# Kernel optimization log

Hardware: AMD Instinct MI355X
Metric: run time of the kernel (lower is better)

## Reference

```python
import jax, jax.numpy as jnp
import numpy as np

N_NODES = 100000

def spmm(rows, cols, vals, x):
    # out[r] = sum_e vals[e] * x[cols[e]] for edges with rows[e] == r
    msgs = vals[:, None] * x[cols]            # [E, F]
    return jax.ops.segment_sum(msgs, rows, num_segments=N_NODES)

def setup_inputs() -> dict:
    key = jax.random.key(0)
    ks = jax.random.split(key, 8)
    N, E, F_IN, H, C = N_NODES, 1600000, 128, 128, 64
    x = jax.random.normal(ks[0], (N, F_IN), dtype=jnp.float32)
    edge_rows = jax.random.randint(ks[1], (E,), 0, N, dtype=jnp.int32)
    edge_cols = jax.random.randint(ks[2], (E,), 0, N, dtype=jnp.int32)
    edge_vals = jax.random.uniform(ks[3], (E,), dtype=jnp.float32)
    W1 = jax.random.normal(ks[4], (F_IN, H), dtype=jnp.float32) * (1.0 / np.sqrt(F_IN))
    b1 = jnp.zeros((H,), dtype=jnp.float32)
    W2 = jax.random.normal(ks[5], (H, C), dtype=jnp.float32) * (1.0 / np.sqrt(H))
    b2 = jnp.zeros((C,), dtype=jnp.float32)
    return {"x": x, "edge_rows": edge_rows, "edge_cols": edge_cols,
            "edge_vals": edge_vals, "W1": W1, "b1": b1, "W2": W2, "b2": b2}

def reference(x, edge_rows, edge_cols, edge_vals, W1, b1, W2, b2):
    # Layer 1: spmm(adj, x) then linear, then ReLU (dropout = identity at eval)
    h = spmm(edge_rows, edge_cols, edge_vals, x)   # [N, F_IN]
    h = h @ W1 + b1                                # [N, H]
    h = jax.nn.relu(h)
    # Layer 2
    h = spmm(edge_rows, edge_cols, edge_vals, h)   # [N, H]
    return h @ W2 + b2                             # [N, C]
```

## Files before the change

### kernel.cpp

```cpp
#include <hip/hip_runtime.h>


typedef __attribute__((ext_vector_type(8))) short short8;
typedef __attribute__((ext_vector_type(4))) float floatx4;
typedef __attribute__((ext_vector_type(2))) float floatx2;

#define ELLS 64
#define RW   256
#define CH   4096
#define EPT  16
#define MAXB 400
#define SLP  68

static __device__ __forceinline__ unsigned short f2bf(float f) {
    unsigned int u = __builtin_bit_cast(unsigned int, f);
    u += 0x7fffu + ((u >> 16) & 1u);
    return (unsigned short)(u >> 16);
}
static __device__ __forceinline__ float bflo(unsigned int u) {
    return __builtin_bit_cast(float, u << 16);
}
static __device__ __forceinline__ float bfhi(unsigned int u) {
    return __builtin_bit_cast(float, u & 0xffff0000u);
}
static __device__ __forceinline__ float slotval(unsigned int s) {
    return (float)(s >> 17) * (1.0f / 32767.0f);
}

__global__ __launch_bounds__(256) void prep_kernel(
    const float* __restrict__ W1, const float* __restrict__ W2,
    unsigned short* __restrict__ W1t, unsigned short* __restrict__ W2t)
{
    int idx = blockIdx.x * 256 + threadIdx.x;
    if (idx < 128 * 128) {
        int n = idx >> 7, k = idx & 127;
        W1t[idx] = f2bf(W1[(size_t)k * 128 + n]);
    }
    if (idx < 64 * 128) {
        int n = idx >> 7, k = idx & 127;
        W2t[idx] = f2bf(W2[(size_t)k * 64 + n]);
    }
}

static __device__ __forceinline__ void gemm1_body(
    const float* __restrict__ A, const unsigned short* __restrict__ Wt,
    unsigned short* __restrict__ Ys, int NP, int N, int bid)
{
    const int lane = threadIdx.x & 63;
    const int wave = threadIdx.x >> 6;
    const int quad = lane >> 4;
    const int l16  = lane & 15;
    const int row0 = bid * 64 + wave * 16;
    int arow = row0 + l16;
    if (arow > N - 1) arow = N - 1;

    short8 af[4];
    const float* ap = A + (size_t)arow * 128 + quad * 8;
    #pragma unroll
    for (int kt = 0; kt < 4; ++kt) {
        const floatx4* p = (const floatx4*)(ap + kt * 32);
        floatx4 lo = __builtin_nontemporal_load(p);
        floatx4 hi = __builtin_nontemporal_load(p + 1);
        short8 t;
        t[0] = (short)f2bf(lo[0]); t[1] = (short)f2bf(lo[1]);
        t[2] = (short)f2bf(lo[2]); t[3] = (short)f2bf(lo[3]);
        t[4] = (short)f2bf(hi[0]); t[5] = (short)f2bf(hi[1]);
        t[6] = (short)f2bf(hi[2]); t[7] = (short)f2bf(hi[3]);
        af[kt] = t;
    }

    floatx4 acc[8];
    #pragma unroll
    for (int nt = 0; nt < 8; ++nt) acc[nt] = (floatx4){0.f, 0.f, 0.f, 0.f};

    #pragma unroll
    for (int nt = 0; nt < 8; ++nt) {
        const unsigned short* wp = Wt + (size_t)(nt * 16 + l16) * 128 + quad * 8;
        #pragma unroll
        for (int kt = 0; kt < 4; ++kt) {
            short8 bfr = *(const short8*)(wp + kt * 32);
            acc[nt] = __builtin_amdgcn_mfma_f32_16x16x32_bf16(
                af[kt], bfr, acc[nt], 0, 0, 0);
        }
    }

    #pragma unroll
    for (int nt = 0; nt < 8; ++nt) {
        #pragma unroll
        for (int r = 0; r < 4; ++r) {
            int row = row0 + quad * 4 + r;
            if (row < N)
                Ys[(size_t)nt * NP * 16 + (size_t)row * 16 + l16] =
                    f2bf(acc[nt][r]);
        }
    }
}

__global__ __launch_bounds__(256) void binA_gemm1_fused(
    const int* __restrict__ erow, const int* __restrict__ ecol,
    const float* __restrict__ eval,
    uint2* __restrict__ slab, unsigned int* __restrict__ offsT,
    int E, int NC, int NB,
    const float* __restrict__ x, const unsigned short* __restrict__ W1t,
    unsigned short* __restrict__ y1s, int NP, int N)
{
    __shared__ unsigned int hist[MAXB + 1];
    __shared__ uint2 compact[CH];

    if ((int)blockIdx.x < NC) {
        const int t     = threadIdx.x;
        const int chunk = blockIdx.x;

        for (int i = t; i <= NB; i += 256) hist[i] = 0;
        __syncthreads();

        int base = chunk * CH + t * EPT;
        unsigned int w0[EPT];
        unsigned int vb[EPT];
        int bk[EPT], rk[EPT];

        if (base + EPT <= E) {
            #pragma unroll
            for (int q = 0; q < 4; ++q) {
                int4   r4 = *(const int4*)(erow + base + q * 4);
                int4   c4 = *(const int4*)(ecol + base + q * 4);
                float4 v4 = *(const float4*)(eval + base + q * 4);
                int rr[4]   = {r4.x, r4.y, r4.z, r4.w};
                int cc[4]   = {c4.x, c4.y, c4.z, c4.w};
                float vv[4] = {v4.x, v4.y, v4.z, v4.w};
                #pragma unroll
                for (int j = 0; j < 4; ++j) {
                    int i = q * 4 + j;
                    bk[i] = rr[j] >> 8;
                    w0[i] = (unsigned int)cc[j]
                          | (((unsigned int)rr[j] & (RW - 1)) << 17);
                    vb[i] = __builtin_bit_cast(unsigned int, vv[j]);
                }
            }
        } else {
            #pragma unroll
            for (int j = 0; j < EPT; ++j) {
                int e = base + j;
                if (e < E) {
                    int r = erow[e];
                    bk[j] = r >> 8;
                    w0[j] = (unsigned int)ecol[e]
                          | (((unsigned int)r & (RW - 1)) << 17);
                    vb[j] = __builtin_bit_cast(unsigned int, eval[e]);
                } else {
                    bk[j] = NB;
                    w0[j] = 0u; vb[j] = 0u;
                }
            }
        }

        #pragma unroll
        for (int j = 0; j < EPT; ++j)
            rk[j] = (int)atomicAdd(&hist[bk[j]], 1u);
        __syncthreads();

        if (t == 0) {
            unsigned int run = 0;
            for (int i = 0; i <= NB; ++i) {
                unsigned int c = hist[i];
                hist[i] = run;
                run += c;
            }
        }
        __syncthreads();

        #pragma unroll
        for (int j = 0; j < EPT; ++j) {
            unsigned int pos = hist[bk[j]] + (unsigned int)rk[j];
            uint2 e; e.x = w0[j]; e.y = vb[j];
            compact[pos] = e;
        }
        __syncthreads();

        uint2* sp = slab + (size_t)chunk * CH;
        #pragma unroll
        for (int s = 0; s < EPT; ++s)
            sp[s * 256 + t] = compact[s * 256 + t];
        unsigned int* op = offsT + (size_t)chunk * (NB + 1);
        for (int i = t; i <= NB; i += 256) op[i] = hist[i];
    } else {
        gemm1_body(x, W1t, y1s, NP, N, blockIdx.x - NC);
    }
}

__global__ __launch_bounds__(256) void binB(
    const uint2* __restrict__ slab, const unsigned int* __restrict__ offsT,
    unsigned int* __restrict__ ell, int* __restrict__ deg,
    int NC, int NB, int N)
{
    __shared__ unsigned int ell_lds[RW * ELLS];
    __shared__ unsigned int cur[RW];

    const int t = threadIdx.x;
    const int b = blockIdx.x;

    for (int i = t; i < RW; i += 256) cur[i] = 0;
    __syncthreads();

    const int grp = t >> 5;
    const int sl  = t & 31;
    for (int cbase = 0; cbase < NC; cbase += 8) {
        int c = cbase + grp;
        if (c < NC) {
            const unsigned int* op = offsT + (size_t)c * (NB + 1) + b;
            unsigned int off = op[0];
            unsigned int end = op[1];
            const uint2* sp = slab + (size_t)c * CH;
            for (unsigned int i = off + (unsigned)sl; i < end; i += 32) {
                uint2 e = sp[i];
                unsigned int rin = e.x >> 17;
                unsigned int col = e.x & 0x1FFFFu;
                float v = __builtin_bit_cast(float, e.y);
                unsigned int q = (unsigned int)(int)(v * 32767.f + 0.5f);
                unsigned int p = atomicAdd(&cur[rin], 1u);
                if (p < ELLS)
                    ell_lds[rin * ELLS + p] = col | (q << 17);
            }
        }
    }
    __syncthreads();

    const uint4* src = (const uint4*)ell_lds;
    uint4* dst = (uint4*)(ell + (size_t)b * RW * ELLS);
    #pragma unroll
    for (int s = 0; s < (RW * ELLS / 4) / 256; ++s)
        dst[s * 256 + t] = src[s * 256 + t];

    int row = b * RW + t;
    if (row < N) deg[row] = min((int)cur[t], ELLS);
}

__global__ __launch_bounds__(256) void spmm1_sliced(
    const int* __restrict__ deg, const unsigned int* __restrict__ ell,
    const unsigned short* __restrict__ y1s, const float* __restrict__ b1,
    unsigned short* __restrict__ h2s, int NP, int N)
{
    __shared__ unsigned int slds[4 * 16 * SLP];

    const int slice = blockIdx.x & 7;
    const int rblk  = blockIdx.x >> 3;
    const int wave  = threadIdx.x >> 6;
    const int lane  = threadIdx.x & 63;
    const int r     = lane >> 2;
    const int fl    = lane & 3;
    const int rbase = rblk * 64 + wave * 16;
    const int row   = rbase + r;

    unsigned int* sw = slds + wave * (16 * SLP);
    const uint4* gp = (const uint4*)(ell + (size_t)rbase * ELLS);
    #pragma unroll
    for (int t = 0; t < 4; ++t) {
        uint4 q = gp[t * 64 + lane];
        int linear = t * 256 + lane * 4;
        int rr = linear >> 6, ii = linear & 63;
        *(uint4*)(sw + rr * SLP + ii) = q;
    }

    int rc = (row < N) ? row : 0;
    int d  = deg[rc];
    if (row >= N) d = 0;

    int dm = d;
    dm = max(dm, __shfl_xor(dm, 4));
    dm = max(dm, __shfl_xor(dm, 8));
    dm = max(dm, __shfl_xor(dm, 16));
    dm = max(dm, __shfl_xor(dm, 32));
    int dm4 = (dm + 3) & ~3;

    const unsigned int* xu = (const unsigned int*)y1s + (size_t)slice * NP * 8;
    const unsigned int* sr = sw + r * SLP;
    float a0 = 0.f, a1 = 0.f, a2 = 0.f, a3 = 0.f;

    for (int i = 0; i < dm4; i += 4) {
        uint4 q = *(const uint4*)(sr + i);
        unsigned int s[4] = {q.x, q.y, q.z, q.w};
        uint2 u[4];
        #pragma unroll
        for (int j = 0; j < 4; ++j) {
            s[j] = (i + j < d) ? s[j] : 0u;
            u[j] = *((const uint2*)(xu + (s[j] & 0x1FFFFu) * 8) + fl);
        }
        #pragma unroll
        for (int j = 0; j < 4; ++j) {
            float v = slotval(s[j]);
            a0 = fmaf(v, bflo(u[j].x), a0);
            a1 = fmaf(v, bfhi(u[j].x), a1);
            a2 = fmaf(v, bflo(u[j].y), a2);
            a3 = fmaf(v, bfhi(u[j].y), a3);
        }
    }

    if (row < N) {
        float4 b = ((const float4*)b1)[slice * 4 + fl];
        unsigned int p0 = (unsigned int)f2bf(fmaxf(a0 + b.x, 0.f))
                        | ((unsigned int)f2bf(fmaxf(a1 + b.y, 0.f)) << 16);
        unsigned int p1 = (unsigned int)f2bf(fmaxf(a2 + b.z, 0.f))
                        | ((unsigned int)f2bf(fmaxf(a3 + b.w, 0.f)) << 16);
        uint2 o; o.x = p0; o.y = p1;
        *(uint2*)((unsigned int*)h2s + (size_t)slice * NP * 8
                  + (size_t)row * 8 + fl * 2) = o;
    }
}

__global__ __launch_bounds__(256) void gemm2_kernel(
    const unsigned short* __restrict__ h2s,
    const unsigned short* __restrict__ W2t,
    unsigned short* __restrict__ y2s, int NP, int N)
{
    const int lane = threadIdx.x & 63;
    const int wave = threadIdx.x >> 6;
    const int quad = lane >> 4;
    const int l16  = lane & 15;
    const int row0 = blockIdx.x * 64 + wave * 16;
    int arow = row0 + l16;
    if (arow > N - 1) arow = N - 1;

    short8 af[4];
    #pragma unroll
    for (int kt = 0; kt < 4; ++kt) {
        int slice = kt * 2 + (quad >> 1);
        af[kt] = *(const short8*)(h2s + (size_t)slice * NP * 16
                                  + (size_t)arow * 16 + (quad & 1) * 8);
    }

    floatx4 acc[4];
    #pragma unroll
    for (int nt = 0; nt < 4; ++nt) acc[nt] = (floatx4){0.f, 0.f, 0.f, 0.f};

    #pragma unroll
    for (int nt = 0; nt < 4; ++nt) {
        const unsigned short* wp = W2t + (size_t)(nt * 16 + l16) * 128 + quad * 8;
        #pragma unroll
        for (int kt = 0; kt < 4; ++kt) {
            short8 bfr = *(const short8*)(wp + kt * 32);
            acc[nt] = __builtin_amdgcn_mfma_f32_16x16x32_bf16(
                af[kt], bfr, acc[nt], 0, 0, 0);
        }
    }

    #pragma unroll
    for (int nt = 0; nt < 4; ++nt) {
        #pragma unroll
        for (int r = 0; r < 4; ++r) {
            int row = row0 + quad * 4 + r;
            if (row < N)
                y2s[(size_t)nt * NP * 16 + (size_t)row * 16 + l16] =
                    f2bf(acc[nt][r]);
        }
    }
}

__global__ __launch_bounds__(256) void spmm2_sliced(
    const int* __restrict__ deg, const unsigned int* __restrict__ ell,
    const unsigned short* __restrict__ y2s, const float* __restrict__ b2,
    float* __restrict__ out, int NP, int N)
{
    __shared__ unsigned int slds[4 * 16 * SLP];

    const int slice = blockIdx.x & 3;
    const int rblk  = blockIdx.x >> 2;
    const int wave  = threadIdx.x >> 6;
    const int lane  = threadIdx.x & 63;
    const int r     = lane >> 2;
    const int fl    = lane & 3;
    const int rbase = rblk * 64 + wave * 16;
    const int row   = rbase + r;

    unsigned int* sw = slds + wave * (16 * SLP);
    const uint4* gp = (const uint4*)(ell + (size_t)rbase * ELLS);
    #pragma unroll
    for (int t = 0; t < 4; ++t) {
        uint4 q = gp[t * 64 + lane];
        int linear = t * 256 + lane * 4;
        int rr = linear >> 6, ii = linear & 63;
        *(uint4*)(sw + rr * SLP + ii) = q;
    }

    int rc = (row < N) ? row : 0;
    int d  = deg[rc];
    if (row >= N) d = 0;

    int dm = d;
    dm = max(dm, __shfl_xor(dm, 4));
    dm = max(dm, __shfl_xor(dm, 8));
    dm = max(dm, __shfl_xor(dm, 16));
    dm = max(dm, __shfl_xor(dm, 32));
    int dm4 = (dm + 3) & ~3;

    const unsigned int* xu = (const unsigned int*)y2s + (size_t)slice * NP * 8;
    const unsigned int* sr = sw + r * SLP;
    float a0 = 0.f, a1 = 0.f, a2 = 0.f, a3 = 0.f;

    for (int i = 0; i < dm4; i += 4) {
        uint4 q = *(const uint4*)(sr + i);
        unsigned int s[4] = {q.x, q.y, q.z, q.w};
        uint2 u[4];
        #pragma unroll
        for (int j = 0; j < 4; ++j) {
            s[j] = (i + j < d) ? s[j] : 0u;
            u[j] = *((const uint2*)(xu + (s[j] & 0x1FFFFu) * 8) + fl);
        }
        #pragma unroll
        for (int j = 0; j < 4; ++j) {
            float v = slotval(s[j]);
            a0 = fmaf(v, bflo(u[j].x), a0);
            a1 = fmaf(v, bfhi(u[j].x), a1);
            a2 = fmaf(v, bflo(u[j].y), a2);
            a3 = fmaf(v, bfhi(u[j].y), a3);
        }
    }

    if (row < N) {
        float4 b = ((const float4*)b2)[slice * 4 + fl];
        floatx4 o;
        o[0] = a0 + b.x; o[1] = a1 + b.y; o[2] = a2 + b.z; o[3] = a3 + b.w;
        __builtin_nontemporal_store(
            o, (floatx4*)(out + (size_t)row * 64 + slice * 16 + fl * 4));
    }
}

extern "C" void kernel_launch(void* const* d_in, const int* in_sizes, int n_in,
                              void* d_out, int out_size, void* d_ws, size_t ws_size,
                              hipStream_t stream)
{
    const float* x    = (const float*)d_in[0];
    const int*   erow = (const int*)  d_in[1];
    const int*   ecol = (const int*)  d_in[2];
    const float* eval = (const float*)d_in[3];
    const float* W1   = (const float*)d_in[4];
    const float* b1   = (const float*)d_in[5];
    const float* W2   = (const float*)d_in[6];
    const float* b2   = (const float*)d_in[7];
    float*       out  = (float*)d_out;

    const int N = in_sizes[0] / 128;
    const int E = in_sizes[1];
    const int NP = N + 128;
    const int NB = (N + RW - 1) / RW;
    const int NC = (E + CH - 1) / CH;

    unsigned short* y1s = (unsigned short*)d_ws;
    unsigned short* h2s = y1s + (size_t)NP * 128;
    unsigned short* W1t = h2s + (size_t)NP * 128;
    unsigned short* W2t = W1t + 128 * 128;
    unsigned int* ell   = (unsigned int*)(W2t + 64 * 128);
    uint2* slab         = (uint2*)(ell + (size_t)NB * RW * ELLS);
    unsigned int* offsT = (unsigned int*)(slab + (size_t)NC * CH);
    int* deg            = (int*)(offsT + (size_t)NC * (NB + 1));
    unsigned short* y2s = (unsigned short*)slab;

    const int mfma_blocks = (N + 63) / 64;
    const int prep_blocks = (128 * 128 + 255) / 256;
    const int rtiles      = (N + 63) / 64;
    const int s1_blocks   = rtiles * 8;
    const int s2_blocks   = rtiles * 4;

    prep_kernel<<<prep_blocks, 256, 0, stream>>>(W1, W2, W1t, W2t);

    binA_gemm1_fused<<<NC + mfma_blocks, 256, 0, stream>>>(
        erow, ecol, eval, slab, offsT, E, NC, NB, x, W1t, y1s, NP, N);

    binB<<<NB, 256, 0, stream>>>(slab, offsT, ell, deg, NC, NB, N);

    spmm1_sliced<<<s1_blocks, 256, 0, stream>>>(
        deg, ell, y1s, b1, h2s, NP, N);

    gemm2_kernel<<<mfma_blocks, 256, 0, stream>>>(h2s, W2t, y2s, NP, N);

    spmm2_sliced<<<s2_blocks, 256, 0, stream>>>(
        deg, ell, y2s, b2, out, NP, N);
}
```

Baseline: 328.1 us.

## Store ELL in interleaved 16-row groups and precompute per-group max degree

binB now writes the ELL slots in a layout where, for each group of 16 rows, the 4-slot blocks of all 16 rows sit next to each other. An LDS bank swizzle keeps the transposing copy conflict-free. binB also writes the per-group maximum degree, so the SpMM kernels can read their index vectors straight from global memory with coalesced uint4 loads. This removes the LDS staging, the full 64-slot preload and the shuffle reductions. In exchange, index loads are now issued inside the loop rather than prefetched, and dmax needs extra workspace after deg.

```diff
diff --git a/kernel.cpp b/kernel.cpp
--- a/kernel.cpp
+++ b/kernel.cpp
@@ -10,7 +10,6 @@
 #define CH   4096
 #define EPT  16
 #define MAXB 400
-#define SLP  68
 
 static __device__ __forceinline__ unsigned short f2bf(float f) {
     unsigned int u = __builtin_bit_cast(unsigned int, f);
@@ -191,7 +190,7 @@
 __global__ __launch_bounds__(256) void binB(
     const uint2* __restrict__ slab, const unsigned int* __restrict__ offsT,
     unsigned int* __restrict__ ell, int* __restrict__ deg,
-    int NC, int NB, int N)
+    int* __restrict__ dmax, int NC, int NB, int N)
 {
     __shared__ unsigned int ell_lds[RW * ELLS];
     __shared__ unsigned int cur[RW];
@@ -218,71 +217,65 @@
                 float v = __builtin_bit_cast(float, e.y);
                 unsigned int q = (unsigned int)(int)(v * 32767.f + 0.5f);
                 unsigned int p = atomicAdd(&cur[rin], 1u);
-                if (p < ELLS)
-                    ell_lds[rin * ELLS + p] = col | (q << 17);
+                if (p < ELLS) {
+                    unsigned int blk = ((p >> 2) + rin) & 15u;
+                    ell_lds[rin * ELLS + blk * 4 + (p & 3)] = col | (q << 17);
+                }
             }
         }
     }
     __syncthreads();
 
-    const uint4* src = (const uint4*)ell_lds;
     uint4* dst = (uint4*)(ell + (size_t)b * RW * ELLS);
-    #pragma unroll
-    for (int s = 0; s < (RW * ELLS / 4) / 256; ++s)
-        dst[s * 256 + t] = src[s * 256 + t];
+    const int s4 = t >> 4;
+    const int r  = t & 15;
+    #pragma unroll
+    for (int s = 0; s < 16; ++s) {
+        unsigned int sblk = (unsigned)((s4 + r) & 15);
+        uint4 q = *(const uint4*)(ell_lds + ((s * 16 + r) * ELLS + sblk * 4));
+        dst[s * 256 + s4 * 16 + r] = q;
+    }
 
     int row = b * RW + t;
     if (row < N) deg[row] = min((int)cur[t], ELLS);
+    if (t < 16) {
+        int m = 0;
+        #pragma unroll
+        for (int i = 0; i < 16; ++i)
+            m = max(m, (int)cur[t * 16 + i]);
+        dmax[b * 16 + t] = min(m, ELLS);
+    }
 }
 
 __global__ __launch_bounds__(256) void spmm1_sliced(
-    const int* __restrict__ deg, const unsigned int* __restrict__ ell,
+    const int* __restrict__ deg, const int* __restrict__ dmax,
+    const unsigned int* __restrict__ ell,
     const unsigned short* __restrict__ y1s, const float* __restrict__ b1,
     unsigned short* __restrict__ h2s, int NP, int N)
 {
-    __shared__ unsigned int slds[4 * 16 * SLP];
-
     const int slice = blockIdx.x & 7;
     const int rblk  = blockIdx.x >> 3;
     const int wave  = threadIdx.x >> 6;
     const int lane  = threadIdx.x & 63;
     const int r     = lane >> 2;
     const int fl    = lane & 3;
-    const int rbase = rblk * 64 + wave * 16;
-    const int row   = rbase + r;
-
-    unsigned int* sw = slds + wave * (16 * SLP);
-    const uint4* gp = (const uint4*)(ell + (size_t)rbase * ELLS);
-    #pragma unroll
-    for (int t = 0; t < 4; ++t) {
-        uint4 q = gp[t * 64 + lane];
-        int linear = t * 256 + lane * 4;
-        int rr = linear >> 6, ii = linear & 63;
-        *(uint4*)(sw + rr * SLP + ii) = q;
-    }
-
-    int rc = (row < N) ? row : 0;
-    int d  = deg[rc];
-    if (row >= N) d = 0;
-
-    int dm = d;
-    dm = max(dm, __shfl_xor(dm, 4));
-    dm = max(dm, __shfl_xor(dm, 8));
-    dm = max(dm, __shfl_xor(dm, 16));
-    dm = max(dm, __shfl_xor(dm, 32));
-    int dm4 = (dm + 3) & ~3;
-
+    const int g     = rblk * 4 + wave;
+    const int row   = g * 16 + r;
+
+    int d  = (row < N) ? deg[row] : 0;
+    int nb = (dmax[g] + 3) >> 2;
+
+    const uint4* eg = (const uint4*)ell + (size_t)g * 256;
     const unsigned int* xu = (const unsigned int*)y1s + (size_t)slice * NP * 8;
-    const unsigned int* sr = sw + r * SLP;
+
     float a0 = 0.f, a1 = 0.f, a2 = 0.f, a3 = 0.f;
-
-    for (int i = 0; i < dm4; i += 4) {
-        uint4 q = *(const uint4*)(sr + i);
+    for (int i4 = 0; i4 < nb; ++i4) {
+        uint4 q = eg[i4 * 16 + r];
         unsigned int s[4] = {q.x, q.y, q.z, q.w};
         uint2 u[4];
         #pragma unroll
         for (int j = 0; j < 4; ++j) {
-            s[j] = (i + j < d) ? s[j] : 0u;
+            s[j] = (i4 * 4 + j < d) ? s[j] : 0u;
             u[j] = *((const uint2*)(xu + (s[j] & 0x1FFFFu) * 8) + fl);
         }
         #pragma unroll
@@ -356,53 +349,34 @@
 }
 
 __global__ __launch_bounds__(256) void spmm2_sliced(
-    const int* __restrict__ deg, const unsigned int* __restrict__ ell,
+    const int* __restrict__ deg, const int* __restrict__ dmax,
+    const unsigned int* __restrict__ ell,
     const unsigned short* __restrict__ y2s, const float* __restrict__ b2,
     float* __restrict__ out, int NP, int N)
 {
-    __shared__ unsigned int slds[4 * 16 * SLP];
-
     const int slice = blockIdx.x & 3;
     const int rblk  = blockIdx.x >> 2;
     const int wave  = threadIdx.x >> 6;
     const int lane  = threadIdx.x & 63;
     const int r     = lane >> 2;
     const int fl    = lane & 3;
-    const int rbase = rblk * 64 + wave * 16;
-    const int row   = rbase + r;
-
-    unsigned int* sw = slds + wave * (16 * SLP);
-    const uint4* gp = (const uint4*)(ell + (size_t)rbase * ELLS);
-    #pragma unroll
-    for (int t = 0; t < 4; ++t) {
-        uint4 q = gp[t * 64 + lane];
-        int linear = t * 256 + lane * 4;
-        int rr = linear >> 6, ii = linear & 63;
-        *(uint4*)(sw + rr * SLP + ii) = q;
-    }
-
-    int rc = (row < N) ? row : 0;
-    int d  = deg[rc];
-    if (row >= N) d = 0;
-
-    int dm = d;
-    dm = max(dm, __shfl_xor(dm, 4));
-    dm = max(dm, __shfl_xor(dm, 8));
-    dm = max(dm, __shfl_xor(dm, 16));
-    dm = max(dm, __shfl_xor(dm, 32));
-    int dm4 = (dm + 3) & ~3;
-
+    const int g     = rblk * 4 + wave;
+    const int row   = g * 16 + r;
+
+    int d  = (row < N) ? deg[row] : 0;
+    int nb = (dmax[g] + 3) >> 2;
+
+    const uint4* eg = (const uint4*)ell + (size_t)g * 256;
     const unsigned int* xu = (const unsigned int*)y2s + (size_t)slice * NP * 8;
-    const unsigned int* sr = sw + r * SLP;
+
     float a0 = 0.f, a1 = 0.f, a2 = 0.f, a3 = 0.f;
-
-    for (int i = 0; i < dm4; i += 4) {
-        uint4 q = *(const uint4*)(sr + i);
+    for (int i4 = 0; i4 < nb; ++i4) {
+        uint4 q = eg[i4 * 16 + r];
         unsigned int s[4] = {q.x, q.y, q.z, q.w};
         uint2 u[4];
         #pragma unroll
         for (int j = 0; j < 4; ++j) {
-            s[j] = (i + j < d) ? s[j] : 0u;
+            s[j] = (i4 * 4 + j < d) ? s[j] : 0u;
             u[j] = *((const uint2*)(xu + (s[j] & 0x1FFFFu) * 8) + fl);
         }
         #pragma unroll
@@ -452,6 +426,7 @@
     uint2* slab         = (uint2*)(ell + (size_t)NB * RW * ELLS);
     unsigned int* offsT = (unsigned int*)(slab + (size_t)NC * CH);
     int* deg            = (int*)(offsT + (size_t)NC * (NB + 1));
+    int* dmax           = deg + N;
     unsigned short* y2s = (unsigned short*)slab;
 
     const int mfma_blocks = (N + 63) / 64;
@@ -465,13 +440,13 @@
     binA_gemm1_fused<<<NC + mfma_blocks, 256, 0, stream>>>(
         erow, ecol, eval, slab, offsT, E, NC, NB, x, W1t, y1s, NP, N);
 
-    binB<<<NB, 256, 0, stream>>>(slab, offsT, ell, deg, NC, NB, N);
+    binB<<<NB, 256, 0, stream>>>(slab, offsT, ell, deg, dmax, NC, NB, N);
 
     spmm1_sliced<<<s1_blocks, 256, 0, stream>>>(
-        deg, ell, y1s, b1, h2s, NP, N);
+        deg, dmax, ell, y1s, b1, h2s, NP, N);
 
     gemm2_kernel<<<mfma_blocks, 256, 0, stream>>>(h2s, W2t, y2s, NP, N);
 
     spmm2_sliced<<<s2_blocks, 256, 0, stream>>>(
-        deg, ell, y2s, b2, out, NP, N);
-}
+        deg, dmax, ell, y2s, b2, out, NP, N);
+}
```

Measured after the change: 316.7 us. 1.04x faster.
